# Kernel optimization log

Hardware: AMD Instinct MI355X
Metric: run time of the kernel (lower is better)

The kernel has to match this reference:

```python
import jax, jax.numpy as jnp
import numpy as np

B, L, D, H = 4, 1024, 1024, 16
DH = D // H
NEG = -1e9
EPS = 1e-5


def setup_inputs() -> dict:
    key = jax.random.key(0)
    ks = jax.random.split(key, 12)
    s = 1.0 / np.sqrt(D)
    inp = {
        "Q": jax.random.normal(ks[0], (B, L, D), jnp.float32),
        "K": jax.random.normal(ks[1], (B, L, D), jnp.float32),
        "V": jax.random.normal(ks[2], (B, L, D), jnp.float32),
        "K_mask": jnp.ones((B, L), jnp.int32),
        "WQ": jax.random.normal(ks[3], (D, D), jnp.float32) * s,
        "bQ": jnp.zeros((D,), jnp.float32),
        "WK": jax.random.normal(ks[4], (D, D), jnp.float32) * s,
        "bK": jnp.zeros((D,), jnp.float32),
        "WV": jax.random.normal(ks[5], (D, D), jnp.float32) * s,
        "bV": jnp.zeros((D,), jnp.float32),
        "WO": jax.random.normal(ks[6], (D, D), jnp.float32) * s,
        "bO": jnp.zeros((D,), jnp.float32),
        "ln_g": jnp.ones((D,), jnp.float32),
        "ln_b": jnp.zeros((D,), jnp.float32),
    }
    return inp


def _mha(Q, K, V, K_mask, WQ, bQ, WK, bK, WV, bV, WO, bO, ln_g, ln_b):
    # projections  [B,L,D]
    q = Q @ WQ + bQ
    k = K @ WK + bK
    v = V @ WV + bV
    # split heads -> [B,H,L,dh]
    q = q.reshape(B, L, H, DH).transpose(0, 2, 1, 3)
    k = k.reshape(B, L, H, DH).transpose(0, 2, 1, 3)
    v = v.reshape(B, L, H, DH).transpose(0, 2, 1, 3)
    # scaled dot product, masked softmax over keys
    scores = jnp.einsum("bhqd,bhkd->bhqk", q, k) / jnp.sqrt(jnp.float32(DH))
    mask = (K_mask > 0)[:, None, None, :]  # [B,1,1,Lk]
    scores = jnp.where(mask, scores, NEG)
    attn = jax.nn.softmax(scores, axis=-1)  # dropout is identity at inference
    ctx = jnp.einsum("bhqk,bhkd->bhqd", attn, v)
    ctx = ctx.transpose(0, 2, 1, 3).reshape(B, L, D)
    # output layer: dense + residual + layernorm
    out = ctx @ WO + bO
    x = out + Q
    mu = jnp.mean(x, axis=-1, keepdims=True)
    var = jnp.var(x, axis=-1, keepdims=True)
    return (x - mu) * jax.lax.rsqrt(var + EPS) * ln_g + ln_b


def reference(Q, K, V, K_mask, WQ, bQ, WK, bK, WV, bV, WO, bO, ln_g, ln_b):
    return _mha(Q, K, V, K_mask, WQ, bQ, WK, bK, WV, bV, WO, bO, ln_g, ln_b)
```

## Files before the change

### kernel.cpp

```cpp
#include <hip/hip_runtime.h>
#include <hip/hip_bf16.h>
#include <stdint.h>

#define Bn 4
#define Ln 1024
#define Dn 1024
#define Hn 16
#define DHn 64
#define Mn (Bn*Ln)

typedef __attribute__((ext_vector_type(8))) short short8v;
typedef __attribute__((ext_vector_type(4))) float floatx4;

__device__ __forceinline__ unsigned short f2b(float f){
  union { float f; unsigned u; } v; v.f = f;
  unsigned r = (v.u + 0x7FFFu + ((v.u >> 16) & 1u)) >> 16;
  return (unsigned short)r;
}
__device__ __forceinline__ unsigned short f2b_fast(float f){
  __hip_bfloat16 h = __float2bfloat16(f);
  return *reinterpret_cast<unsigned short*>(&h);
}

typedef const unsigned __attribute__((address_space(1)))* gas1_t;
typedef unsigned __attribute__((address_space(3)))* las3_t;
__device__ __forceinline__ void gload16(const void* g, void* l){
  __builtin_amdgcn_global_load_lds((gas1_t)(uintptr_t)g, (las3_t)(uintptr_t)l, 16, 0, 0);
}

__global__ __launch_bounds__(256) void prep_k(const float* __restrict__ W0,
    const float* __restrict__ W1, const float* __restrict__ W2,
    const float* __restrict__ W3, unsigned short* __restrict__ Wt0,
    unsigned short* __restrict__ Wt1, unsigned short* __restrict__ Wt2,
    unsigned short* __restrict__ Wt3, const float* __restrict__ x0,
    const float* __restrict__ x1, const float* __restrict__ x2,
    unsigned short* __restrict__ o0, unsigned short* __restrict__ o1,
    unsigned short* __restrict__ o2)
{
  __shared__ float tile[64][65];
  if (blockIdx.x < 1024){
    const int z = blockIdx.x >> 8, rem = blockIdx.x & 255;
    const float* W; unsigned short* Wt;
    switch (z){
      case 0: W = W0; Wt = Wt0; break;
      case 1: W = W1; Wt = Wt1; break;
      case 2: W = W2; Wt = Wt2; break;
      default: W = W3; Wt = Wt3; break;
    }
    const int nb = (rem & 15) * 64, kb = (rem >> 4) * 64;
    const int tx = threadIdx.x & 63, ty = threadIdx.x >> 6;
    #pragma unroll
    for (int r = 0; r < 64; r += 4)
      tile[r + ty][tx] = W[(size_t)(kb + r + ty) * 1024 + nb + tx];
    __syncthreads();
    #pragma unroll
    for (int r = 0; r < 64; r += 4)
      Wt[(size_t)(nb + r + ty) * 1024 + kb + tx] = f2b(tile[tx][r + ty]);
  } else {
    const int i = (blockIdx.x - 1024) * 256 + threadIdx.x;
    const int sel = i >> 20, idx = i & 0xFFFFF;
    const float* x = sel == 0 ? x0 : (sel == 1 ? x1 : x2);
    unsigned short* o = sel == 0 ? o0 : (sel == 1 ? o1 : o2);
    float4 v = reinterpret_cast<const float4*>(x)[idx];
    union { unsigned short u[4]; uint2 q; } p;
    p.u[0] = f2b(v.x); p.u[1] = f2b(v.y); p.u[2] = f2b(v.z); p.u[3] = f2b(v.w);
    reinterpret_cast<uint2*>(o)[idx] = p.q;
  }
}

template<int MODE>
__device__ __forceinline__ void gemm8_core(const unsigned short* __restrict__ Ab,
    const unsigned short* __restrict__ Btp, const float* __restrict__ bias,
    void* __restrict__ outp, float scale, unsigned short* lds, int nt, int mt)
{
  const int tid = threadIdx.x;
  const int lane = tid & 63, wave = tid >> 6;
  const int wr = wave >> 2, wc = wave & 3;
  const int lg = lane >> 4, lr = lane & 15;
  const int m0 = mt * 256, n0 = nt * 256;

  const unsigned short* gAb[2];
  const unsigned short* gBb[2];
  int ldso[2];
  #pragma unroll
  for (int i = 0; i < 2; i++){
    int c = tid + 512 * i;
    int g16 = c >> 6, lrr = c & 15, lgg = (c >> 4) & 3;
    int row = g16 * 16 + lrr;
    gAb[i] = Ab  + (size_t)(m0 + row) * 1024 + lgg * 8;
    gBb[i] = Btp + (size_t)(n0 + row) * 1024 + lgg * 8;
    ldso[i] = c * 8;
  }
  auto stageA = [&](int sg){
    unsigned short* slot = lds + (sg & 3) * 16384;
    const int kcol = (sg >> 1) * 64 + (sg & 1) * 32;
    #pragma unroll
    for (int i = 0; i < 2; i++) gload16(gAb[i] + kcol, &slot[ldso[i]]);
  };
  auto stageB = [&](int sg){
    unsigned short* slot = lds + (sg & 3) * 16384 + 8192;
    const int kcol = (sg >> 1) * 64 + (sg & 1) * 32;
    #pragma unroll
    for (int i = 0; i < 2; i++) gload16(gBb[i] + kcol, &slot[ldso[i]]);
  };

  floatx4 acc[8][4] = {};

  stageA(0); stageB(0); stageA(1); stageB(1); stageA(2); stageB(2);

  for (int t = 0; t < 16; t++){
    unsigned short* slot0 = lds + ((2 * t) & 3) * 16384;
    unsigned short* slot1 = lds + ((2 * t + 1) & 3) * 16384;
    short8v af[4], bf[4];
    if (t < 15) asm volatile("s_waitcnt vmcnt(4)" ::: "memory");
    else        asm volatile("s_waitcnt vmcnt(0)" ::: "memory");
    __builtin_amdgcn_s_barrier();
    __builtin_amdgcn_sched_barrier(0);
    if (t < 15) stageA(2 * t + 3);
    #pragma unroll
    for (int n = 0; n < 4; n++)
      bf[n] = *reinterpret_cast<const short8v*>(&slot0[8192 + ((wc * 4 + n) * 64 + lane) * 8]);
    #pragma unroll
    for (int i2 = 0; i2 < 4; i2++)
      af[i2] = *reinterpret_cast<const short8v*>(&slot0[((wr * 8 + i2) * 64 + lane) * 8]);
    __builtin_amdgcn_s_setprio(1);
    #pragma unroll
    for (int a = 0; a < 4; a++)
      #pragma unroll
      for (int n = 0; n < 4; n++)
        acc[a][n] = __builtin_amdgcn_mfma_f32_16x16x32_bf16(af[a], bf[n], acc[a][n], 0, 0, 0);
    __builtin_amdgcn_s_setprio(0);
    if (t < 15) stageB(2 * t + 3);
    #pragma unroll
    for (int i2 = 0; i2 < 4; i2++)
      af[i2] = *reinterpret_cast<const short8v*>(&slot0[((wr * 8 + 4 + i2) * 64 + lane) * 8]);
    __builtin_amdgcn_s_setprio(1);
    #pragma unroll
    for (int a = 0; a < 4; a++)
      #pragma unroll
      for (int n = 0; n < 4; n++)
        acc[4 + a][n] = __builtin_amdgcn_mfma_f32_16x16x32_bf16(af[a], bf[n], acc[4 + a][n], 0, 0, 0);
    __builtin_amdgcn_s_setprio(0);
    __builtin_amdgcn_sched_barrier(0);
    __builtin_amdgcn_s_barrier();
    __builtin_amdgcn_sched_barrier(0);
    if (t < 14) stageA(2 * t + 4);
    #pragma unroll
    for (int n = 0; n < 4; n++)
      bf[n] = *reinterpret_cast<const short8v*>(&slot1[8192 + ((wc * 4 + n) * 64 + lane) * 8]);
    #pragma unroll
    for (int i2 = 0; i2 < 4; i2++)
      af[i2] = *reinterpret_cast<const short8v*>(&slot1[((wr * 8 + i2) * 64 + lane) * 8]);
    __builtin_amdgcn_s_setprio(1);
    #pragma unroll
    for (int a = 0; a < 4; a++)
      #pragma unroll
      for (int n = 0; n < 4; n++)
        acc[a][n] = __builtin_amdgcn_mfma_f32_16x16x32_bf16(af[a], bf[n], acc[a][n], 0, 0, 0);
    __builtin_amdgcn_s_setprio(0);
    if (t < 14) stageB(2 * t + 4);
    #pragma unroll
    for (int i2 = 0; i2 < 4; i2++)
      af[i2] = *reinterpret_cast<const short8v*>(&slot1[((wr * 8 + 4 + i2) * 64 + lane) * 8]);
    __builtin_amdgcn_s_setprio(1);
    #pragma unroll
    for (int a = 0; a < 4; a++)
      #pragma unroll
      for (int n = 0; n < 4; n++)
        acc[4 + a][n] = __builtin_amdgcn_mfma_f32_16x16x32_bf16(af[a], bf[n], acc[4 + a][n], 0, 0, 0);
    __builtin_amdgcn_s_setprio(0);
    __builtin_amdgcn_sched_barrier(0);
  }

  if constexpr (MODE == 2){
    __syncthreads();
    #pragma unroll
    for (int n = 0; n < 4; n++){
      const int gn_l = wc * 64 + n * 16 + lr;
      const float bb = bias[n0 + gn_l];
      const int X = (gn_l & 7) << 3;
      #pragma unroll
      for (int a = 0; a < 8; a++){
        const int gm_l = wr * 128 + a * 16 + lg * 4;
        union { unsigned short u[4]; uint2 q; } pk;
        #pragma unroll
        for (int r = 0; r < 4; r++) pk.u[r] = f2b((acc[a][n][r] + bb) * scale);
        *reinterpret_cast<uint2*>(&lds[gn_l * 256 + (gm_l ^ X)]) = pk.q;
      }
    }
    __syncthreads();
    const int bb2 = m0 >> 10, l0 = m0 & 1023;
    const int row = tid >> 1, colb = (tid & 1) * 128;
    const int h2 = (n0 + row) >> 6, d = (n0 + row) & 63;
    unsigned short* obase = (unsigned short*)outp +
        (((size_t)(bb2 * Hn + h2)) * DHn + d) * Ln + l0 + colb;
    const int XR = (row & 7) << 3;
    #pragma unroll
    for (int g = 0; g < 16; g++){
      short8v v = *reinterpret_cast<const short8v*>(&lds[row * 256 + ((colb + g * 8) ^ XR)]);
      *reinterpret_cast<short8v*>(obase + g * 8) = v;
    }
  } else {
    unsigned short* plw = lds + wave * 1152;
    unsigned short* o = (unsigned short*)outp;
    const int gnb = n0 + wc * 64;
    const int h2 = gnb >> 6;
    float bb4[4];
    #pragma unroll
    for (int n = 0; n < 4; n++) bb4[n] = bias[gnb + n * 16 + lr];
    #pragma unroll
    for (int a = 0; a < 8; a++){
      #pragma unroll
      for (int n = 0; n < 4; n++)
        #pragma unroll
        for (int r = 0; r < 4; r++)
          plw[(lg * 4 + r) * 72 + n * 16 + lr] = f2b((acc[a][n][r] + bb4[n]) * scale);
      #pragma unroll
      for (int it = 0; it < 2; it++){
        const int row = it * 8 + (lane >> 3);
        const int c   = lane & 7;
        const int gm  = m0 + wr * 128 + a * 16 + row;
        const int b2 = gm >> 10, l = gm & 1023;
        short8v v = *reinterpret_cast<const short8v*>(&plw[row * 72 + c * 8]);
        *reinterpret_cast<short8v*>(o + (((size_t)(b2 * Hn + h2)) * Ln + l) * DHn + c * 8) = v;
      }
    }
  }
}

__global__ __launch_bounds__(512, 2) void gemmqkv8_k(
    const unsigned short* __restrict__ A0, const unsigned short* __restrict__ A1,
    const unsigned short* __restrict__ A2, const unsigned short* __restrict__ W0,
    const unsigned short* __restrict__ W1, const unsigned short* __restrict__ W2,
    const float* __restrict__ b0, const float* __restrict__ b1,
    const float* __restrict__ b2, unsigned short* __restrict__ o0,
    unsigned short* __restrict__ o1, unsigned short* __restrict__ o2, float qscl)
{
  __shared__ __align__(16) unsigned short lds[65536];
  const int g = blockIdx.x >> 3;
  const int nt = g & 3;
  const int panel = (g >> 2) * 8 + (blockIdx.x & 7);
  const int z = panel >> 4, mt = panel & 15;
  if (z == 0)
    gemm8_core<0>(A0, W0, b0, o0, qscl, lds, nt, mt);
  else if (z == 1)
    gemm8_core<0>(A1, W1, b1, o1, 1.f, lds, nt, mt);
  else
    gemm8_core<2>(A2, W2, b2, o2, 1.f, lds, nt, mt);
}

__global__ __launch_bounds__(256) void gemmo_k(const unsigned short* __restrict__ Ab,
    const unsigned short* __restrict__ W, const float* __restrict__ bias,
    float* __restrict__ out, const float* __restrict__ resid)
{
  __shared__ __align__(16) unsigned short lds[32768];
  const int bid = blockIdx.x;
  const int xcd = bid & 7, k = bid >> 3;
  const int mt = xcd * 4 + (k >> 3);
  const int nt = k & 7;

  const int tid = threadIdx.x;
  const int lane = tid & 63, wave = tid >> 6;
  const int wr = wave >> 1, wc = wave & 1;
  const int lg = lane >> 4, lr = lane & 15;
  const int m0 = mt * 128, n0 = nt * 128;

  const unsigned short* gA[2];
  const unsigned short* gB[2];
  int ldso[2];
  #pragma unroll
  for (int i = 0; i < 2; i++){
    int c = tid + 256 * i;
    int g16 = c >> 6, lrr = c & 15, lgg = (c >> 4) & 3;
    int row = g16 * 16 + lrr;
    gA[i] = Ab + (size_t)(m0 + row) * 1024 + lgg * 8;
    gB[i] = W  + (size_t)(n0 + row) * 1024 + lgg * 8;
    ldso[i] = c * 8;
  }
  auto issue = [&](int s){
    unsigned short* base = lds + (s & 3) * 8192;
    const int kc = s * 32;
    #pragma unroll
    for (int i = 0; i < 2; i++) gload16(gA[i] + kc, &base[ldso[i]]);
    #pragma unroll
    for (int i = 0; i < 2; i++) gload16(gB[i] + kc, &base[4096 + ldso[i]]);
  };

  floatx4 acc[4][4] = {};

  issue(0); issue(1); issue(2);

  for (int s = 0; s < 32; s++){
    unsigned short* base = lds + (s & 3) * 8192;
    if (s <= 29)      asm volatile("s_waitcnt vmcnt(8)" ::: "memory");
    else if (s == 30) asm volatile("s_waitcnt vmcnt(4)" ::: "memory");
    else              asm volatile("s_waitcnt vmcnt(0)" ::: "memory");
    __builtin_amdgcn_s_barrier();
    __builtin_amdgcn_sched_barrier(0);
    if (s <= 28) issue(s + 3);
    short8v af[4], bf[4];
    #pragma unroll
    for (int m = 0; m < 4; m++)
      af[m] = *reinterpret_cast<const short8v*>(&base[((wr * 4 + m) * 64 + lane) * 8]);
    #pragma unroll
    for (int n = 0; n < 4; n++)
      bf[n] = *reinterpret_cast<const short8v*>(&base[4096 + ((wc * 4 + n) * 64 + lane) * 8]);
    __builtin_amdgcn_s_setprio(1);
    #pragma unroll
    for (int m = 0; m < 4; m++)
      #pragma unroll
      for (int n = 0; n < 4; n++)
        acc[m][n] = __builtin_amdgcn_mfma_f32_16x16x32_bf16(af[m], bf[n], acc[m][n], 0, 0, 0);
    __builtin_amdgcn_s_setprio(0);
    __builtin_amdgcn_sched_barrier(0);
  }

  #pragma unroll
  for (int n = 0; n < 4; n++){
    const int gn = n0 + wc * 64 + n * 16 + lr;
    const float bb = bias[gn];
    #pragma unroll
    for (int m = 0; m < 4; m++){
      const int gm0 = m0 + wr * 64 + m * 16 + lg * 4;
      #pragma unroll
      for (int r = 0; r < 4; r++){
        const int gm = gm0 + r;
        out[(size_t)gm * Dn + gn] = acc[m][n][r] + bb + resid[(size_t)gm * Dn + gn];
      }
    }
  }
}

__global__ __launch_bounds__(256) void attn_k(const unsigned short* __restrict__ qb,
    const unsigned short* __restrict__ kbf, const unsigned short* __restrict__ vtb,
    const int* __restrict__ kmask, unsigned short* __restrict__ ctx)
{
  const int bh = blockIdx.x;
  const int qt = blockIdx.y;
  const int b = bh >> 4, h = bh & 15;
  const int tid = threadIdx.x;
  const int w = tid >> 6, lane = tid & 63;
  const int lg = lane >> 4, lr = lane & 15;

  const unsigned short* qp = qb  + (size_t)bh * Ln * DHn;
  const unsigned short* kp = kbf + (size_t)bh * Ln * DHn;
  const unsigned short* vp = vtb + (size_t)bh * DHn * Ln;
  const int q0 = qt * 128 + w * 32;

  __shared__ __align__(16) unsigned short ldsK[3][4096];
  __shared__ __align__(16) unsigned short ldsV[3][4096];
  __shared__ __align__(16) unsigned short plds[4][32][72];
  __shared__ __align__(16) int ldsM[1024];

  short8v aq[2][2];
  #pragma unroll
  for (int f = 0; f < 2; f++)
    #pragma unroll
    for (int ks = 0; ks < 2; ks++)
      aq[f][ks] = *reinterpret_cast<const short8v*>(
          qp + (size_t)(q0 + f * 16 + lr) * DHn + ks * 32 + lg * 8);

  const unsigned short* gK[2];
  const unsigned short* gV[2];
  #pragma unroll
  for (int i = 0; i < 2; i++){
    int bc = w * 2 + i;
    int ks = bc >> 2, j = bc & 3;
    int row = j * 16 + lr, col = ks * 32 + lg * 8;
    gK[i] = kp + (size_t)row * DHn + col;
    gV[i] = vp + (size_t)row * Ln  + col;
  }
  auto issue = [&](int t){
    unsigned short* bK = ldsK[t % 3];
    unsigned short* bV = ldsV[t % 3];
    #pragma unroll
    for (int i = 0; i < 2; i++){
      gload16(gK[i] + (size_t)t * 4096, &bK[(w * 2 + i) * 512]);
      gload16(gV[i] + (size_t)t * 64,   &bV[(w * 2 + i) * 512]);
    }
  };

  floatx4 accO[2][4] = {};
  float lsacc[2][4] = {{0.f,0.f,0.f,0.f},{0.f,0.f,0.f,0.f}};

  gload16(kmask + b * Ln + w * 256 + lane * 4, &ldsM[w * 256]);
  issue(0);
  issue(1);

  for (int t = 0; t < 16; t++){
    if (t < 15) asm volatile("s_waitcnt vmcnt(4)" ::: "memory");
    else        asm volatile("s_waitcnt vmcnt(0)" ::: "memory");
    __builtin_amdgcn_s_barrier();
    __builtin_amdgcn_sched_barrier(0);
    if (t < 14) issue(t + 2);

    const unsigned short* bK = ldsK[t % 3];
    const unsigned short* bV = ldsV[t % 3];

    floatx4 s[2][4] = {};
    #pragma unroll
    for (int ks = 0; ks < 2; ks++)
      #pragma unroll
      for (int j = 0; j < 4; j++){
        short8v bk = *reinterpret_cast<const short8v*>(&bK[((ks * 4 + j) * 64 + lane) * 8]);
        s[0][j] = __builtin_amdgcn_mfma_f32_16x16x32_bf16(aq[0][ks], bk, s[0][j], 0, 0, 0);
        s[1][j] = __builtin_amdgcn_mfma_f32_16x16x32_bf16(aq[1][ks], bk, s[1][j], 0, 0, 0);
      }
    int mk[4];
    #pragma unroll
    for (int j = 0; j < 4; j++) mk[j] = ldsM[t * 64 + j * 16 + lr];
    if (__all(mk[0] > 0 && mk[1] > 0 && mk[2] > 0 && mk[3] > 0)){
      #pragma unroll
      for (int f = 0; f < 2; f++)
        #pragma unroll
        for (int j = 0; j < 4; j++)
          #pragma unroll
          for (int r = 0; r < 4; r++){
            float p = __builtin_amdgcn_exp2f(s[f][j][r]);
            lsacc[f][r] += p;
            plds[w][f * 16 + lg * 4 + r][j * 16 + lr] = f2b_fast(p);
          }
    } else {
      #pragma unroll
      for (int j = 0; j < 4; j++){
        const float madd = mk[j] > 0 ? 0.f : -1e9f;
        #pragma unroll
        for (int f = 0; f < 2; f++)
          #pragma unroll
          for (int r = 0; r < 4; r++){
            float p = __builtin_amdgcn_exp2f(s[f][j][r] + madd);
            lsacc[f][r] += p;
            plds[w][f * 16 + lg * 4 + r][j * 16 + lr] = f2b_fast(p);
          }
      }
    }
    #pragma unroll
    for (int ks = 0; ks < 2; ks++){
      short8v pa0 = *reinterpret_cast<const short8v*>(&plds[w][lr][ks * 32 + lg * 8]);
      short8v pa1 = *reinterpret_cast<const short8v*>(&plds[w][16 + lr][ks * 32 + lg * 8]);
      #pragma unroll
      for (int n = 0; n < 4; n++){
        short8v bv = *reinterpret_cast<const short8v*>(&bV[((ks * 4 + n) * 64 + lane) * 8]);
        accO[0][n] = __builtin_amdgcn_mfma_f32_16x16x32_bf16(pa0, bv, accO[0][n], 0, 0, 0);
        accO[1][n] = __builtin_amdgcn_mfma_f32_16x16x32_bf16(pa1, bv, accO[1][n], 0, 0, 0);
      }
    }
  }

  #pragma unroll
  for (int f = 0; f < 2; f++)
    #pragma unroll
    for (int r = 0; r < 4; r++){
      lsacc[f][r] += __shfl_xor(lsacc[f][r], 1, 64);
      lsacc[f][r] += __shfl_xor(lsacc[f][r], 2, 64);
      lsacc[f][r] += __shfl_xor(lsacc[f][r], 4, 64);
      lsacc[f][r] += __shfl_xor(lsacc[f][r], 8, 64);
      lsacc[f][r] = 1.f / fmaxf(lsacc[f][r], 1e-20f);
    }
  #pragma unroll
  for (int f = 0; f < 2; f++)
    #pragma unroll
    for (int n = 0; n < 4; n++)
      #pragma unroll
      for (int r = 0; r < 4; r++)
        plds[w][f * 16 + lg * 4 + r][n * 16 + lr] = f2b_fast(accO[f][n][r] * lsacc[f][r]);
  #pragma unroll
  for (int it = 0; it < 4; it++){
    const int row = it * 8 + (lane >> 3);
    const int c = lane & 7;
    const int q = q0 + row;
    short8v v = *reinterpret_cast<const short8v*>(&plds[w][row][c * 8]);
    *reinterpret_cast<short8v*>(ctx + ((size_t)(b * Ln + q)) * Dn + h * DHn + c * 8) = v;
  }
}

__global__ __launch_bounds__(256) void ln_k(const float* __restrict__ x,
    const float* __restrict__ g, const float* __restrict__ bt, float* __restrict__ out)
{
  const int row = blockIdx.x;
  const int tid = threadIdx.x;
  float4 v = *reinterpret_cast<const float4*>(x + (size_t)row * 1024 + tid * 4);
  float s  = v.x + v.y + v.z + v.w;
  float sq = v.x * v.x + v.y * v.y + v.z * v.z + v.w * v.w;
  #pragma unroll
  for (int off = 32; off >= 1; off >>= 1){
    s  += __shfl_xor(s, off, 64);
    sq += __shfl_xor(sq, off, 64);
  }
  __shared__ float psm[4], pqm[4];
  const int w = tid >> 6;
  if ((tid & 63) == 0){ psm[w] = s; pqm[w] = sq; }
  __syncthreads();
  s  = psm[0] + psm[1] + psm[2] + psm[3];
  sq = pqm[0] + pqm[1] + pqm[2] + pqm[3];
  const float mean = s * (1.f / 1024.f);
  const float var  = sq * (1.f / 1024.f) - mean * mean;
  const float inv  = rsqrtf(var + 1e-5f);
  float4 gg = *reinterpret_cast<const float4*>(g  + tid * 4);
  float4 bb = *reinterpret_cast<const float4*>(bt + tid * 4);
  float4 o;
  o.x = (v.x - mean) * inv * gg.x + bb.x;
  o.y = (v.y - mean) * inv * gg.y + bb.y;
  o.z = (v.z - mean) * inv * gg.z + bb.z;
  o.w = (v.w - mean) * inv * gg.w + bb.w;
  *reinterpret_cast<float4*>(out + (size_t)row * 1024 + tid * 4) = o;
}

extern "C" void kernel_launch(void* const* d_in, const int* in_sizes, int n_in,
                              void* d_out, int out_size, void* d_ws, size_t ws_size,
                              hipStream_t stream)
{
  const float* Qin = (const float*)d_in[0];
  const float* Kin = (const float*)d_in[1];
  const float* Vin = (const float*)d_in[2];
  const int*   Kms = (const int*)d_in[3];
  const float* WQ  = (const float*)d_in[4];
  const float* bQ  = (const float*)d_in[5];
  const float* WK  = (const float*)d_in[6];
  const float* bK  = (const float*)d_in[7];
  const float* WV  = (const float*)d_in[8];
  const float* bV  = (const float*)d_in[9];
  const float* WO  = (const float*)d_in[10];
  const float* bO  = (const float*)d_in[11];
  const float* lng = (const float*)d_in[12];
  const float* lnb = (const float*)d_in[13];

  char* ws = (char*)d_ws;
  const size_t MB = 1024u * 1024u;
  unsigned short* wqt = (unsigned short*)(ws + 0 * MB);
  unsigned short* wkt = (unsigned short*)(ws + 2 * MB);
  unsigned short* wvt = (unsigned short*)(ws + 4 * MB);
  unsigned short* wot = (unsigned short*)(ws + 6 * MB);
  unsigned short* qbf = (unsigned short*)(ws + 8 * MB);
  unsigned short* kbf = (unsigned short*)(ws + 16 * MB);
  unsigned short* vtb = (unsigned short*)(ws + 24 * MB);
  unsigned short* ctx = (unsigned short*)(ws + 32 * MB);
  float*          xbf = (float*)(ws + 40 * MB);
  unsigned short* cv0 = (unsigned short*)(ws + 32 * MB);
  unsigned short* cv1 = (unsigned short*)(ws + 40 * MB);
  unsigned short* cv2 = (unsigned short*)(ws + 48 * MB);

  dim3 blk(256);
  prep_k<<<13312, blk, 0, stream>>>(WQ, WK, WV, WO, wqt, wkt, wvt, wot,
                                    Qin, Kin, Vin, cv0, cv1, cv2);

  const float QSCL = 0.125f * 1.44269504088896f;
  gemmqkv8_k<<<192, dim3(512), 0, stream>>>(cv0, cv1, cv2, wqt, wkt, wvt,
                                            bQ, bK, bV, qbf, kbf, vtb, QSCL);

  attn_k<<<dim3(64, 8), blk, 0, stream>>>(qbf, kbf, vtb, Kms, ctx);

  gemmo_k<<<256, blk, 0, stream>>>(ctx, wot, bO, xbf, Qin);

  ln_k<<<4096, blk, 0, stream>>>(xbf, lng, lnb, (float*)d_out);
}
```

Baseline: 119.7 us.

## Store pre-LayerNorm activations as bf16 via LDS-staged coalesced writes; deepen QKV GEMM waits

The output-projection GEMM now writes residual-added activations as bf16 rather than fp32. It stages each 16-row tile through LDS so rows go out as coalesced 16-byte stores, and the LayerNorm kernel reads bf16 back. This halves the intermediate traffic between the two kernels and replaces scattered scalar stores. It costs precision in the pre-normalization values. Separately, the QKV GEMM uses looser vmcnt waits and adds a second wait before the mid-iteration barrier, to keep more loads in flight.

```diff
diff --git a/kernel.cpp b/kernel.cpp
--- a/kernel.cpp
+++ b/kernel.cpp
@@ -20,6 +20,9 @@
 __device__ __forceinline__ unsigned short f2b_fast(float f){
   __hip_bfloat16 h = __float2bfloat16(f);
   return *reinterpret_cast<unsigned short*>(&h);
+}
+__device__ __forceinline__ float b2f(unsigned short u){
+  union { unsigned u; float f; } v; v.u = (unsigned)u << 16; return v.f;
 }
 
 typedef const unsigned __attribute__((address_space(1)))* gas1_t;
@@ -112,8 +115,8 @@
     unsigned short* slot0 = lds + ((2 * t) & 3) * 16384;
     unsigned short* slot1 = lds + ((2 * t + 1) & 3) * 16384;
     short8v af[4], bf[4];
-    if (t < 15) asm volatile("s_waitcnt vmcnt(4)" ::: "memory");
-    else        asm volatile("s_waitcnt vmcnt(0)" ::: "memory");
+    if (t < 15) asm volatile("s_waitcnt vmcnt(8)" ::: "memory");
+    else        asm volatile("s_waitcnt vmcnt(4)" ::: "memory");
     __builtin_amdgcn_s_barrier();
     __builtin_amdgcn_sched_barrier(0);
     if (t < 15) stageA(2 * t + 3);
@@ -142,6 +145,8 @@
         acc[4 + a][n] = __builtin_amdgcn_mfma_f32_16x16x32_bf16(af[a], bf[n], acc[4 + a][n], 0, 0, 0);
     __builtin_amdgcn_s_setprio(0);
     __builtin_amdgcn_sched_barrier(0);
+    if (t < 15) asm volatile("s_waitcnt vmcnt(8)" ::: "memory");
+    else        asm volatile("s_waitcnt vmcnt(0)" ::: "memory");
     __builtin_amdgcn_s_barrier();
     __builtin_amdgcn_sched_barrier(0);
     if (t < 14) stageA(2 * t + 4);
@@ -251,7 +256,7 @@
 
 __global__ __launch_bounds__(256) void gemmo_k(const unsigned short* __restrict__ Ab,
     const unsigned short* __restrict__ W, const float* __restrict__ bias,
-    float* __restrict__ out, const float* __restrict__ resid)
+    unsigned short* __restrict__ out, const float* __restrict__ resid)
 {
   __shared__ __align__(16) unsigned short lds[32768];
   const int bid = blockIdx.x;
@@ -315,18 +320,29 @@
     __builtin_amdgcn_sched_barrier(0);
   }
 
-  #pragma unroll
-  for (int n = 0; n < 4; n++){
-    const int gn = n0 + wc * 64 + n * 16 + lr;
-    const float bb = bias[gn];
-    #pragma unroll
-    for (int m = 0; m < 4; m++){
-      const int gm0 = m0 + wr * 64 + m * 16 + lg * 4;
+  unsigned short* plw = lds + wave * 1152;
+  float bb4[4];
+  #pragma unroll
+  for (int n = 0; n < 4; n++) bb4[n] = bias[n0 + wc * 64 + n * 16 + lr];
+  #pragma unroll
+  for (int m = 0; m < 4; m++){
+    #pragma unroll
+    for (int n = 0; n < 4; n++){
+      const int gn = n0 + wc * 64 + n * 16 + lr;
       #pragma unroll
       for (int r = 0; r < 4; r++){
-        const int gm = gm0 + r;
-        out[(size_t)gm * Dn + gn] = acc[m][n][r] + bb + resid[(size_t)gm * Dn + gn];
+        const int gm = m0 + wr * 64 + m * 16 + lg * 4 + r;
+        float v = acc[m][n][r] + bb4[n] + resid[(size_t)gm * Dn + gn];
+        plw[(lg * 4 + r) * 72 + n * 16 + lr] = f2b_fast(v);
       }
+    }
+    #pragma unroll
+    for (int it = 0; it < 2; it++){
+      const int row = it * 8 + (lane >> 3);
+      const int c = lane & 7;
+      const int gm = m0 + wr * 64 + m * 16 + row;
+      short8v v = *reinterpret_cast<const short8v*>(&plw[row * 72 + c * 8]);
+      *reinterpret_cast<short8v*>(out + (size_t)gm * Dn + n0 + wc * 64 + c * 8) = v;
     }
   }
 }
@@ -474,14 +490,18 @@
   }
 }
 
-__global__ __launch_bounds__(256) void ln_k(const float* __restrict__ x,
+__global__ __launch_bounds__(256) void ln_k(const unsigned short* __restrict__ x,
     const float* __restrict__ g, const float* __restrict__ bt, float* __restrict__ out)
 {
   const int row = blockIdx.x;
   const int tid = threadIdx.x;
-  float4 v = *reinterpret_cast<const float4*>(x + (size_t)row * 1024 + tid * 4);
-  float s  = v.x + v.y + v.z + v.w;
-  float sq = v.x * v.x + v.y * v.y + v.z * v.z + v.w * v.w;
+  uint2 u = *reinterpret_cast<const uint2*>(x + (size_t)row * 1024 + tid * 4);
+  float v0 = b2f((unsigned short)(u.x & 0xFFFF));
+  float v1 = b2f((unsigned short)(u.x >> 16));
+  float v2 = b2f((unsigned short)(u.y & 0xFFFF));
+  float v3 = b2f((unsigned short)(u.y >> 16));
+  float s  = v0 + v1 + v2 + v3;
+  float sq = v0 * v0 + v1 * v1 + v2 * v2 + v3 * v3;
   #pragma unroll
   for (int off = 32; off >= 1; off >>= 1){
     s  += __shfl_xor(s, off, 64);
@@ -499,10 +519,10 @@
   float4 gg = *reinterpret_cast<const float4*>(g  + tid * 4);
   float4 bb = *reinterpret_cast<const float4*>(bt + tid * 4);
   float4 o;
-  o.x = (v.x - mean) * inv * gg.x + bb.x;
-  o.y = (v.y - mean) * inv * gg.y + bb.y;
-  o.z = (v.z - mean) * inv * gg.z + bb.z;
-  o.w = (v.w - mean) * inv * gg.w + bb.w;
+  o.x = (v0 - mean) * inv * gg.x + bb.x;
+  o.y = (v1 - mean) * inv * gg.y + bb.y;
+  o.z = (v2 - mean) * inv * gg.z + bb.z;
+  o.w = (v3 - mean) * inv * gg.w + bb.w;
   *reinterpret_cast<float4*>(out + (size_t)row * 1024 + tid * 4) = o;
 }
 
@@ -535,7 +555,7 @@
   unsigned short* kbf = (unsigned short*)(ws + 16 * MB);
   unsigned short* vtb = (unsigned short*)(ws + 24 * MB);
   unsigned short* ctx = (unsigned short*)(ws + 32 * MB);
-  float*          xbf = (float*)(ws + 40 * MB);
+  unsigned short* xbh = (unsigned short*)(ws + 40 * MB);
   unsigned short* cv0 = (unsigned short*)(ws + 32 * MB);
   unsigned short* cv1 = (unsigned short*)(ws + 40 * MB);
   unsigned short* cv2 = (unsigned short*)(ws + 48 * MB);
@@ -550,7 +570,7 @@
 
   attn_k<<<dim3(64, 8), blk, 0, stream>>>(qbf, kbf, vtb, Kms, ctx);
 
-  gemmo_k<<<256, blk, 0, stream>>>(ctx, wot, bO, xbf, Qin);
-
-  ln_k<<<4096, blk, 0, stream>>>(xbf, lng, lnb, (float*)d_out);
-}
+  gemmo_k<<<256, blk, 0, stream>>>(ctx, wot, bO, xbh, Qin);
+
+  ln_k<<<4096, blk, 0, stream>>>(xbh, lng, lnb, (float*)d_out);
+}
```

Measured after the change: 117.4 us, median of 5. No clear change (-1.9%).
